# Kernel optimization log

Measured on AMD Instinct MI355X. Metric: run time of the kernel, lower is better.

Reference implementation:

```python
import jax, jax.numpy as jnp
import numpy as np

NEG_SLOPE = 0.01  # F.leaky_relu default
DROP_P = 0.5      # F.dropout(p=0.5, training=True by default in this code)


def _lrelu(x):
    return jnp.where(x >= 0, x, NEG_SLOPE * x)


def _hconv(Xi, X, Ht, Hs, edge_w, theta, w_trans, bias):
    # Faithful to Ht.T @ diag(edge_w) @ Hs @ X @ theta + Xi @ w_trans + bias,
    # with diag(edge_w) fused as a per-row scale of the [E, out] intermediate.
    msg = (Hs @ X) @ theta                 # [E, out]
    agg = Ht.T @ (edge_w[:, None] * msg)   # [N, out]
    return _lrelu(agg + Xi @ w_trans + bias)


def setup_inputs() -> dict:
    key = jax.random.key(0)
    ks = jax.random.split(key, 14)
    N, E, F0, H = 8192, 4096, 128, 128
    f32 = jnp.float32
    return {
        "xi": jax.random.normal(ks[0], (N, F0), f32),
        "x": jax.random.normal(ks[1], (N, F0), f32),
        "Ht": jax.random.uniform(ks[2], (E, N), f32),
        "Hs": jax.random.uniform(ks[3], (E, N), f32),
        "state": jax.random.normal(ks[4], (N, 1), f32),
        # conv0 params (std=0.01 init as in torch code)
        "w_trans0": 0.01 * jax.random.normal(ks[5], (F0, H), f32),
        "theta0": 0.01 * jax.random.normal(ks[6], (F0, H), f32),
        "edge_w0": jnp.ones((E,), f32),
        "bias0": 0.01 * jax.random.normal(ks[7], (H,), f32),
        # conv1 params
        "w_trans1": 0.01 * jax.random.normal(ks[8], (H, H), f32),
        "theta1": 0.01 * jax.random.normal(ks[9], (H, H), f32),
        "edge_w1": jnp.ones((E,), f32),
        "bias1": 0.01 * jax.random.normal(ks[10], (H,), f32),
        # fc: Linear(H+1, 1)
        "fc_w": 0.01 * jax.random.normal(ks[11], (H + 1, 1), f32),
        "fc_b": 0.01 * jax.random.normal(ks[12], (1,), f32),
    }


def reference(xi, x, Ht, Hs, state,
              w_trans0, theta0, edge_w0, bias0,
              w_trans1, theta1, edge_w1, bias1,
              fc_w, fc_b):
    X1 = _hconv(xi, x, Ht, Hs, edge_w0, theta0, w_trans0, bias0)  # [N, H]
    # F.dropout(p=0.5) is active (training=True default); fixed mask for determinism
    keep = jax.random.bernoulli(jax.random.key(42), 1.0 - DROP_P, X1.shape)
    X1 = jnp.where(keep, X1 / (1.0 - DROP_P), 0.0)
    X2 = _hconv(xi, X1, Ht, Hs, edge_w1, theta1, w_trans1, bias1)  # [N, H]
    X = _lrelu(X2)  # second leaky_relu, as in DQN.forward
    Xc = jnp.concatenate([X, state], axis=1)  # [N, H+1]
    return Xc @ fc_w + fc_b  # [N, 1]
```

## Files before the change

kernel.cpp:

```cpp
#include <hip/hip_runtime.h>
#include <stdint.h>


typedef short short8 __attribute__((ext_vector_type(8)));
typedef float f32x4 __attribute__((ext_vector_type(4)));

static constexpr int N = 8192, E = 4096, F = 128;
static constexpr int SA = 16, SB = 8;

#define ASM_VMCNT(n) asm volatile("s_waitcnt vmcnt(" #n ")" ::: "memory")
#define ASM_LGKM0() asm volatile("s_waitcnt lgkmcnt(0)" ::: "memory")

__device__ __forceinline__ void gload_lds16(const short* g, short* l) {
  __builtin_amdgcn_global_load_lds(
      (const __attribute__((address_space(1))) unsigned int*)g,
      (__attribute__((address_space(3))) unsigned int*)l, 16, 0, 0);
}

__device__ __forceinline__ unsigned rotl32(unsigned x, int r) {
  return (x << r) | (x >> (32 - r));
}

__device__ __forceinline__ uint2 threefry2x32(unsigned k0, unsigned k1,
                                              unsigned x0, unsigned x1) {
  unsigned ks[3] = {k0, k1, k0 ^ k1 ^ 0x1BD11BDAu};
  x0 += ks[0];
  x1 += ks[1];
  const int R0[4] = {13, 15, 26, 6};
  const int R1[4] = {17, 29, 16, 24};
#pragma unroll
  for (int i = 0; i < 5; ++i) {
#pragma unroll
    for (int j = 0; j < 4; ++j) {
      const int r = (i % 2 == 0) ? R0[j] : R1[j];
      x0 += x1;
      x1 = rotl32(x1, r);
      x1 ^= x0;
    }
    x0 += ks[(i + 1) % 3];
    x1 += ks[(i + 2) % 3] + (unsigned)(i + 1);
  }
  return make_uint2(x0, x1);
}

__device__ __forceinline__ float drop_scale(unsigned idx) {
  const uint2 o = threefry2x32(0u, 42u, 0u, idx);
  return ((o.x ^ o.y) & 0x80000000u) ? 0.0f : 2.0f;
}

__device__ __forceinline__ float lrelu(float v) {
  return v >= 0.0f ? v : 0.01f * v;
}

__device__ __forceinline__ unsigned rne1(float a) {
  unsigned ua = __builtin_bit_cast(unsigned, a);
  ua += 0x7fffu + ((ua >> 16) & 1u);
  return ua >> 16;
}
__device__ __forceinline__ float bf16_val(unsigned u16) {
  return __builtin_bit_cast(float, u16 << 16);
}
__device__ __forceinline__ unsigned pk_bf16(float a, float b) {
  return rne1(a) | (rne1(b) << 16);
}
__device__ __forceinline__ void split2(float a, float b, unsigned& hi,
                                       unsigned& lo) {
  const unsigned ha = rne1(a), hb = rne1(b);
  const float ra = a - bf16_val(ha), rb = b - bf16_val(hb);
  hi = ha | (hb << 16);
  lo = rne1(ra) | (rne1(rb) << 16);
}
__device__ __forceinline__ void split1(float a, unsigned& h, unsigned& l) {
  h = rne1(a);
  l = rne1(a - bf16_val(h));
}

template <bool TRANSA>
__global__ __launch_bounds__(512, 4) void big_gemm(
    const float* __restrict__ A, const short* __restrict__ Bhg,
    const short* __restrict__ Blg, float* __restrict__ P, int M, int lda) {
  __shared__ __align__(16) short As[3][4096];
  __shared__ __align__(16) short Bhs[3][4096];
  __shared__ __align__(16) short Bls[3][4096];

  const int tid = threadIdx.x;
  const int lane = tid & 63;
  const int w = tid >> 6;
  const int wm = (w & 3) << 5;
  const int wn = (w >> 2) << 6;
  const int l15 = lane & 15;
  const int q = lane >> 4;
  const int r0 = blockIdx.x * 128;
  constexpr int NT = 16;
  const int kt0 = blockIdx.y * NT;

  const int m0a = tid >> 3;
  const int m0b = (512 + tid) >> 3;
  const int kq0 = tid & 7;
  const int m1 = tid & 127;
  const int eo1 = tid >> 7;

  float Rf[2][8];

  auto loadA = [&](float* R, int kt) {
    if constexpr (!TRANSA) {
      *(float4*)&R[0] =
          *(const float4*)(A + (size_t)(r0 + m0a) * lda + kt * 32 + 4 * kq0);
      *(float4*)&R[4] =
          *(const float4*)(A + (size_t)(r0 + m0b) * lda + kt * 32 + 4 * kq0);
    } else {
#pragma unroll
      for (int r = 0; r < 8; ++r)
        R[r] = A[(size_t)(kt * 32 + 8 * eo1 + r) * lda + r0 + m1];
    }
  };
  auto packA = [&](const float* R, int buf) {
    if constexpr (!TRANSA) {
      const int s0 = (kq0 >> 1) ^ ((m0a >> 1) & 3);
      uint2 u0 = {pk_bf16(R[0], R[1]), pk_bf16(R[2], R[3])};
      *(uint2*)&As[buf][m0a * 32 + s0 * 8 + (kq0 & 1) * 4] = u0;
      const int s1 = (kq0 >> 1) ^ ((m0b >> 1) & 3);
      uint2 u1 = {pk_bf16(R[4], R[5]), pk_bf16(R[6], R[7])};
      *(uint2*)&As[buf][m0b * 32 + s1 * 8 + (kq0 & 1) * 4] = u1;
    } else {
      const int s0 = eo1 ^ ((m1 >> 1) & 3);
      uint4 u = {pk_bf16(R[0], R[1]), pk_bf16(R[2], R[3]),
                 pk_bf16(R[4], R[5]), pk_bf16(R[6], R[7])};
      *(uint4*)&As[buf][m1 * 32 + s0 * 8] = u;
    }
  };
  auto stageB = [&](int buf, int kt) {
    const size_t g = (size_t)kt * 4096 + w * 512 + lane * 8;
    gload_lds16(Bhg + g, &Bhs[buf][w * 512]);
    gload_lds16(Blg + g, &Bls[buf][w * 512]);
  };

  f32x4 acc[2][4];
#pragma unroll
  for (int i = 0; i < 2; ++i)
#pragma unroll
    for (int j = 0; j < 4; ++j) acc[i][j] = (f32x4){0.f, 0.f, 0.f, 0.f};

  loadA(Rf[0], kt0 + 0);
  stageB(0, kt0 + 0);
  loadA(Rf[1], kt0 + 1);
  stageB(1, kt0 + 1);
  if constexpr (!TRANSA) ASM_VMCNT(4); else ASM_VMCNT(10);
  __builtin_amdgcn_sched_barrier(0);
  packA(Rf[0], 0);
  ASM_LGKM0();
  __builtin_amdgcn_s_barrier();

  auto step = [&](int i, float* Ri, float* Rp) {
    const int cur = i % 3, nxt = (i + 1) % 3, nn = (i + 2) % 3;
    if (i + 2 < NT) {
      loadA(Ri, kt0 + i + 2);
      stageB(nn, kt0 + i + 2);
    }
    __builtin_amdgcn_sched_barrier(0);
    short8 af[2], bh[4], bl[4];
#pragma unroll
    for (int ii = 0; ii < 2; ++ii) {
      const int m = wm + 16 * ii + l15;
      af[ii] = *(const short8*)&As[cur][m * 32 + ((q ^ ((m >> 1) & 3)) << 3)];
    }
#pragma unroll
    for (int j = 0; j < 4; ++j) {
      const int c = wn + 16 * j + l15;
      bh[j] = *(const short8*)&Bhs[cur][c * 32 + (q << 3)];
      bl[j] = *(const short8*)&Bls[cur][c * 32 + (q << 3)];
    }
#pragma unroll
    for (int ii = 0; ii < 2; ++ii)
#pragma unroll
      for (int j = 0; j < 4; ++j) {
        acc[ii][j] = __builtin_amdgcn_mfma_f32_16x16x32_bf16(af[ii], bl[j],
                                                             acc[ii][j], 0, 0, 0);
        acc[ii][j] = __builtin_amdgcn_mfma_f32_16x16x32_bf16(af[ii], bh[j],
                                                             acc[ii][j], 0, 0, 0);
      }
    if (i + 1 < NT) {
      if (i + 2 < NT) {
        if constexpr (!TRANSA) ASM_VMCNT(4); else ASM_VMCNT(10);
      } else {
        ASM_VMCNT(0);
      }
      __builtin_amdgcn_sched_barrier(0);
      packA(Rp, nxt);
    }
    ASM_LGKM0();
    __builtin_amdgcn_s_barrier();
  };

  for (int ib = 0; ib < NT; ib += 2) {
    step(ib, Rf[0], Rf[1]);
    step(ib + 1, Rf[1], Rf[0]);
  }

  const int s = blockIdx.y;
  const int rquad = q << 2;
#pragma unroll
  for (int i = 0; i < 2; ++i)
#pragma unroll
    for (int j = 0; j < 4; ++j)
#pragma unroll
      for (int r = 0; r < 4; ++r) {
        const int row = r0 + wm + 16 * i + rquad + r;
        const int col = wn + 16 * j + l15;
        P[((size_t)s * M + row) * 128 + col] = acc[i][j][r];
      }
}

template <bool WA>
__device__ __forceinline__ void small_core(
    const float* __restrict__ src, const float* __restrict__ W,
    const float* __restrict__ bias, float* __restrict__ out,
    short* __restrict__ outH, short* __restrict__ outL, short* WTh, short* WTl,
    short* Xh, short* Xl, int n0, int tid) {
  constexpr int TI = WA ? 4 : 2;
  constexpr int TJ = WA ? 2 : 4;
  const int lane = tid & 63;
  const int w = tid >> 6;
  const int l15 = lane & 15;
  const int wm = (w & 1) * (WA ? 64 : 32);
  const int wn = (w >> 1) * (WA ? 32 : 64);

  f32x4 acc[TI][TJ];
#pragma unroll
  for (int i = 0; i < TI; ++i)
#pragma unroll
    for (int j = 0; j < TJ; ++j) acc[i][j] = (f32x4){0.f, 0.f, 0.f, 0.f};

  for (int k0 = 0; k0 < 128; k0 += 32) {
#pragma unroll
    for (int i = 0; i < 2; ++i) {
      const int f = i * 256 + tid;
      const int c = f & 127;
      const int eo = f >> 7;
      uint4 uh, ul;
      unsigned* ph = (unsigned*)&uh;
      unsigned* pl = (unsigned*)&ul;
#pragma unroll
      for (int r = 0; r < 4; ++r) {
        const float a = W[(size_t)(k0 + 8 * eo + 2 * r) * 128 + c];
        const float b = W[(size_t)(k0 + 8 * eo + 2 * r + 1) * 128 + c];
        split2(a, b, ph[r], pl[r]);
      }
      *(uint4*)&WTh[c * 40 + 8 * eo] = uh;
      *(uint4*)&WTl[c * 40 + 8 * eo] = ul;
    }
#pragma unroll
    for (int i = 0; i < 2; ++i) {
      const int qq = i * 256 + tid;
      const int n = qq >> 3;
      const int kq = qq & 7;
      const float4 v =
          *(const float4*)(src + (size_t)(n0 + n) * 128 + k0 + 4 * kq);
      uint2 uh, ul;
      split2(v.x, v.y, uh.x, ul.x);
      split2(v.z, v.w, uh.y, ul.y);
      *(uint2*)&Xh[n * 40 + 4 * kq] = uh;
      *(uint2*)&Xl[n * 40 + 4 * kq] = ul;
    }
    __syncthreads();

    const int koff = (lane >> 4) << 3;
    short8 ah[TI], al[TI], bh[TJ], bl[TJ];
#pragma unroll
    for (int i = 0; i < TI; ++i) {
      const int m = wm + 16 * i + l15;
      ah[i] = WA ? *(const short8*)&WTh[m * 40 + koff]
                 : *(const short8*)&Xh[m * 40 + koff];
      al[i] = WA ? *(const short8*)&WTl[m * 40 + koff]
                 : *(const short8*)&Xl[m * 40 + koff];
    }
#pragma unroll
    for (int j = 0; j < TJ; ++j) {
      const int c = wn + 16 * j + l15;
      bh[j] = WA ? *(const short8*)&Xh[c * 40 + koff]
                 : *(const short8*)&WTh[c * 40 + koff];
      bl[j] = WA ? *(const short8*)&Xl[c * 40 + koff]
                 : *(const short8*)&WTl[c * 40 + koff];
    }
#pragma unroll
    for (int i = 0; i < TI; ++i)
#pragma unroll
      for (int j = 0; j < TJ; ++j) {
        acc[i][j] = __builtin_amdgcn_mfma_f32_16x16x32_bf16(al[i], bh[j],
                                                            acc[i][j], 0, 0, 0);
        acc[i][j] = __builtin_amdgcn_mfma_f32_16x16x32_bf16(ah[i], bl[j],
                                                            acc[i][j], 0, 0, 0);
        acc[i][j] = __builtin_amdgcn_mfma_f32_16x16x32_bf16(ah[i], bh[j],
                                                            acc[i][j], 0, 0, 0);
      }
    __syncthreads();
  }

  const int rquad = (lane >> 4) << 2;
#pragma unroll
  for (int i = 0; i < TI; ++i)
#pragma unroll
    for (int j = 0; j < TJ; ++j) {
      if constexpr (WA) {
        const int colg = n0 + wn + 16 * j + l15;
        const size_t tb = (size_t)(colg >> 5) * 4096 + (colg & 31);
#pragma unroll
        for (int r = 0; r < 4; ++r) {
          const int row = wm + 16 * i + rquad + r;
          unsigned h, l;
          split1(acc[i][j][r], h, l);
          outH[tb + (size_t)row * 32] = (short)h;
          outL[tb + (size_t)row * 32] = (short)l;
        }
      } else {
#pragma unroll
        for (int r = 0; r < 4; ++r) {
          const int row = wm + 16 * i + rquad + r;
          const int col = wn + 16 * j + l15;
          out[(size_t)(n0 + row) * 128 + col] = acc[i][j][r] + bias[col];
        }
      }
    }
}

__global__ __launch_bounds__(256) void small_fused(
    const float* __restrict__ srcT, const float* __restrict__ Wth,
    const float* __restrict__ srcB, const float* __restrict__ Wwt,
    const float* __restrict__ bias, short* __restrict__ TtH,
    short* __restrict__ TtL, float* __restrict__ Badd) {
  __shared__ __align__(16) short WTh[128 * 40], WTl[128 * 40];
  __shared__ __align__(16) short Xh[64 * 40], Xl[64 * 40];
  const int n0 = blockIdx.x * 64;
  if (blockIdx.y == 0)
    small_core<true>(srcT, Wth, nullptr, nullptr, TtH, TtL, WTh, WTl, Xh, Xl,
                     n0, threadIdx.x);
  else
    small_core<false>(srcB, Wwt, bias, Badd, nullptr, nullptr, WTh, WTl, Xh, Xl,
                      n0, threadIdx.x);
}

__global__ __launch_bounds__(256) void reduce_A(const float* __restrict__ P,
                                                const float* __restrict__ ew,
                                                short* __restrict__ MtH,
                                                short* __restrict__ MtL) {
  __shared__ float Lt[8 * 132];
  const int tid = threadIdx.x;
  const int e0 = blockIdx.x * 8;
  {
    const int el = tid >> 5;
    const int cq = tid & 31;
    float4 a = {0.f, 0.f, 0.f, 0.f};
#pragma unroll
    for (int s = 0; s < SA; ++s) {
      const float4 v =
          *(const float4*)(P + ((size_t)s * E + e0 + el) * 128 + 4 * cq);
      a.x += v.x; a.y += v.y; a.z += v.z; a.w += v.w;
    }
    const float sc = ew[e0 + el];
    a.x *= sc; a.y *= sc; a.z *= sc; a.w *= sc;
    *(float4*)&Lt[el * 132 + 4 * cq] = a;
  }
  __syncthreads();
  {
    const int c = tid >> 1;
    const int eq = tid & 1;
    const int eb = e0 + 4 * eq;
    float4 o;
    o.x = Lt[(4 * eq + 0) * 132 + c];
    o.y = Lt[(4 * eq + 1) * 132 + c];
    o.z = Lt[(4 * eq + 2) * 132 + c];
    o.w = Lt[(4 * eq + 3) * 132 + c];
    uint2 uh, ul;
    split2(o.x, o.y, uh.x, ul.x);
    split2(o.z, o.w, uh.y, ul.y);
    const size_t off = (size_t)(eb >> 5) * 4096 + (size_t)c * 32 + (eb & 31);
    *(uint2*)&MtH[off] = uh;
    *(uint2*)&MtL[off] = ul;
  }
}

__global__ __launch_bounds__(256) void reduce_B1(const float* __restrict__ P,
                                                 const float* __restrict__ Badd,
                                                 float* __restrict__ X1) {
  const int q = blockIdx.x * 256 + threadIdx.x;
  const int n = q >> 5;
  const int cq = q & 31;
  float4 a = {0.f, 0.f, 0.f, 0.f};
#pragma unroll
  for (int s = 0; s < SB; ++s) {
    const float4 v = *(const float4*)(P + ((size_t)s * N + n) * 128 + 4 * cq);
    a.x += v.x; a.y += v.y; a.z += v.z; a.w += v.w;
  }
  const float4 b = *(const float4*)(Badd + (size_t)n * 128 + 4 * cq);
  const unsigned fb = (unsigned)(n * 128 + 4 * cq);
  float4 o;
  o.x = lrelu(a.x + b.x) * drop_scale(fb + 0u);
  o.y = lrelu(a.y + b.y) * drop_scale(fb + 1u);
  o.z = lrelu(a.z + b.z) * drop_scale(fb + 2u);
  o.w = lrelu(a.w + b.w) * drop_scale(fb + 3u);
  *(float4*)&X1[(size_t)n * 128 + 4 * cq] = o;
}

__global__ __launch_bounds__(256) void reduce_B2(
    const float* __restrict__ P, const float* __restrict__ Badd,
    const float* __restrict__ fcw, const float* __restrict__ state,
    const float* __restrict__ fcb, float* __restrict__ out) {
  __shared__ float part[4];
  const int tid = threadIdx.x;
  const int nn = tid >> 7;
  const int c = tid & 127;
  const int n = blockIdx.x * 2 + nn;
  float v = 0.f;
#pragma unroll
  for (int s = 0; s < SB; ++s) v += P[((size_t)s * N + n) * 128 + c];
  v += Badd[(size_t)n * 128 + c];
  float p = lrelu(lrelu(v)) * fcw[c];
#pragma unroll
  for (int m = 32; m >= 1; m >>= 1) p += __shfl_xor(p, m, 64);
  if ((tid & 63) == 0) part[tid >> 6] = p;
  __syncthreads();
  if (tid < 2)
    out[blockIdx.x * 2 + tid] = part[2 * tid] + part[2 * tid + 1] +
                                state[blockIdx.x * 2 + tid] * fcw[128] + fcb[0];
}

extern "C" void kernel_launch(void* const* d_in, const int* in_sizes, int n_in,
                              void* d_out, int out_size, void* d_ws,
                              size_t ws_size, hipStream_t stream) {
  (void)in_sizes; (void)n_in; (void)out_size; (void)ws_size;

  const float* xi = (const float*)d_in[0];
  const float* x = (const float*)d_in[1];
  const float* Ht = (const float*)d_in[2];
  const float* Hs = (const float*)d_in[3];
  const float* state = (const float*)d_in[4];
  const float* wt0 = (const float*)d_in[5];
  const float* th0 = (const float*)d_in[6];
  const float* ew0 = (const float*)d_in[7];
  const float* bi0 = (const float*)d_in[8];
  const float* wt1 = (const float*)d_in[9];
  const float* th1 = (const float*)d_in[10];
  const float* ew1 = (const float*)d_in[11];
  const float* bi1 = (const float*)d_in[12];
  const float* fcw = (const float*)d_in[13];
  const float* fcb = (const float*)d_in[14];
  float* out = (float*)d_out;

  float* ws = (float*)d_ws;
  float* P = ws;
  short* TtH = (short*)(P + (size_t)8388608);
  short* TtL = TtH + (size_t)1048576;
  short* MtH = TtL + (size_t)1048576;
  short* MtL = MtH + (size_t)524288;
  float* Badd = (float*)(MtL + (size_t)524288);
  float* X1 = Badd + (size_t)N * 128;

  small_fused<<<dim3(N / 64, 2), 256, 0, stream>>>(x, th0, xi, wt0, bi0, TtH,
                                                   TtL, Badd);
  big_gemm<false><<<dim3(E / 128, SA), 512, 0, stream>>>(Hs, TtH, TtL, P, E, N);
  reduce_A<<<E / 8, 256, 0, stream>>>(P, ew0, MtH, MtL);
  big_gemm<true><<<dim3(N / 128, SB), 512, 0, stream>>>(Ht, MtH, MtL, P, N, N);
  reduce_B1<<<N * F / 4 / 256, 256, 0, stream>>>(P, Badd, X1);

  small_fused<<<dim3(N / 64, 2), 256, 0, stream>>>(X1, th1, xi, wt1, bi1, TtH,
                                                   TtL, Badd);
  big_gemm<false><<<dim3(E / 128, SA), 512, 0, stream>>>(Hs, TtH, TtL, P, E, N);
  reduce_A<<<E / 8, 256, 0, stream>>>(P, ew1, MtH, MtL);
  big_gemm<true><<<dim3(N / 128, SB), 512, 0, stream>>>(Ht, MtH, MtL, P, N, N);
  reduce_B2<<<N / 2, 256, 0, stream>>>(P, Badd, fcw, state, fcb, out);
}
```

Before: 458.2 us.

## Load A fragments directly into registers and re-layout B tiles by k-quarter

The big GEMM no longer stages the A operand through shared memory. Each lane loads its own fp32 A fragment straight from global memory into a triple-buffered register set and packs it to bf16 just before the MFMAs. This removes the LDS writes, the LDS reads and the lgkmcnt waits for A. The B hi/lo tiles produced by the small kernels are re-laid out so each k-quarter is contiguous, which lets the B fragment reads skip the swizzle. MFMA blocks are wrapped in s_setprio. In exchange it uses more registers, and the uncoalesced transposed-A global loads (8 strided scalar loads per row group) may hurt bandwidth.

```diff
diff --git a/kernel.cpp b/kernel.cpp
--- a/kernel.cpp
+++ b/kernel.cpp
@@ -9,7 +9,6 @@
 static constexpr int SA = 16, SB = 8;
 
 #define ASM_VMCNT(n) asm volatile("s_waitcnt vmcnt(" #n ")" ::: "memory")
-#define ASM_LGKM0() asm volatile("s_waitcnt lgkmcnt(0)" ::: "memory")
 
 __device__ __forceinline__ void gload_lds16(const short* g, short* l) {
   __builtin_amdgcn_global_load_lds(
@@ -79,7 +78,6 @@
 __global__ __launch_bounds__(512, 4) void big_gemm(
     const float* __restrict__ A, const short* __restrict__ Bhg,
     const short* __restrict__ Blg, float* __restrict__ P, int M, int lda) {
-  __shared__ __align__(16) short As[3][4096];
   __shared__ __align__(16) short Bhs[3][4096];
   __shared__ __align__(16) short Bls[3][4096];
 
@@ -94,39 +92,26 @@
   constexpr int NT = 16;
   const int kt0 = blockIdx.y * NT;
 
-  const int m0a = tid >> 3;
-  const int m0b = (512 + tid) >> 3;
-  const int kq0 = tid & 7;
-  const int m1 = tid & 127;
-  const int eo1 = tid >> 7;
-
-  float Rf[2][8];
-
-  auto loadA = [&](float* R, int kt) {
+  const int am0 = wm + l15;
+  const int am1 = wm + 16 + l15;
+
+  float Ra[3][16];
+
+  auto loadA = [&](int set, int kt) {
     if constexpr (!TRANSA) {
-      *(float4*)&R[0] =
-          *(const float4*)(A + (size_t)(r0 + m0a) * lda + kt * 32 + 4 * kq0);
-      *(float4*)&R[4] =
-          *(const float4*)(A + (size_t)(r0 + m0b) * lda + kt * 32 + 4 * kq0);
+      const float* p0 = A + (size_t)(r0 + am0) * lda + kt * 32 + q * 8;
+      const float* p1 = A + (size_t)(r0 + am1) * lda + kt * 32 + q * 8;
+      *(float4*)&Ra[set][0] = *(const float4*)p0;
+      *(float4*)&Ra[set][4] = *(const float4*)(p0 + 4);
+      *(float4*)&Ra[set][8] = *(const float4*)p1;
+      *(float4*)&Ra[set][12] = *(const float4*)(p1 + 4);
     } else {
-#pragma unroll
-      for (int r = 0; r < 8; ++r)
-        R[r] = A[(size_t)(kt * 32 + 8 * eo1 + r) * lda + r0 + m1];
-    }
-  };
-  auto packA = [&](const float* R, int buf) {
-    if constexpr (!TRANSA) {
-      const int s0 = (kq0 >> 1) ^ ((m0a >> 1) & 3);
-      uint2 u0 = {pk_bf16(R[0], R[1]), pk_bf16(R[2], R[3])};
-      *(uint2*)&As[buf][m0a * 32 + s0 * 8 + (kq0 & 1) * 4] = u0;
-      const int s1 = (kq0 >> 1) ^ ((m0b >> 1) & 3);
-      uint2 u1 = {pk_bf16(R[4], R[5]), pk_bf16(R[6], R[7])};
-      *(uint2*)&As[buf][m0b * 32 + s1 * 8 + (kq0 & 1) * 4] = u1;
-    } else {
-      const int s0 = eo1 ^ ((m1 >> 1) & 3);
-      uint4 u = {pk_bf16(R[0], R[1]), pk_bf16(R[2], R[3]),
-                 pk_bf16(R[4], R[5]), pk_bf16(R[6], R[7])};
-      *(uint4*)&As[buf][m1 * 32 + s0 * 8] = u;
+      const float* p0 = A + (size_t)(kt * 32 + q * 8) * lda + r0 + am0;
+#pragma unroll
+      for (int r = 0; r < 8; ++r) Ra[set][r] = p0[(size_t)r * lda];
+      const float* p1 = p0 + 16;
+#pragma unroll
+      for (int r = 0; r < 8; ++r) Ra[set][8 + r] = p1[(size_t)r * lda];
     }
   };
   auto stageB = [&](int buf, int kt) {
@@ -134,6 +119,12 @@
     gload_lds16(Bhg + g, &Bhs[buf][w * 512]);
     gload_lds16(Blg + g, &Bls[buf][w * 512]);
   };
+  auto mk = [&](const float* R) {
+    union { unsigned u[4]; short8 s; } c;
+#pragma unroll
+    for (int t = 0; t < 4; ++t) c.u[t] = pk_bf16(R[2 * t], R[2 * t + 1]);
+    return c.s;
+  };
 
   f32x4 acc[2][4];
 #pragma unroll
@@ -141,60 +132,65 @@
 #pragma unroll
     for (int j = 0; j < 4; ++j) acc[i][j] = (f32x4){0.f, 0.f, 0.f, 0.f};
 
-  loadA(Rf[0], kt0 + 0);
+  loadA(0, kt0 + 0);
   stageB(0, kt0 + 0);
-  loadA(Rf[1], kt0 + 1);
+  loadA(1, kt0 + 1);
   stageB(1, kt0 + 1);
-  if constexpr (!TRANSA) ASM_VMCNT(4); else ASM_VMCNT(10);
+  if constexpr (!TRANSA) ASM_VMCNT(4); else ASM_VMCNT(18);
   __builtin_amdgcn_sched_barrier(0);
-  packA(Rf[0], 0);
-  ASM_LGKM0();
   __builtin_amdgcn_s_barrier();
 
-  auto step = [&](int i, float* Ri, float* Rp) {
-    const int cur = i % 3, nxt = (i + 1) % 3, nn = (i + 2) % 3;
+#pragma unroll
+  for (int i = 0; i < NT; ++i) {
+    const int cur = i % 3;
     if (i + 2 < NT) {
-      loadA(Ri, kt0 + i + 2);
-      stageB(nn, kt0 + i + 2);
+      loadA((i + 2) % 3, kt0 + i + 2);
+      stageB((i + 2) % 3, kt0 + i + 2);
     }
     __builtin_amdgcn_sched_barrier(0);
-    short8 af[2], bh[4], bl[4];
-#pragma unroll
-    for (int ii = 0; ii < 2; ++ii) {
-      const int m = wm + 16 * ii + l15;
-      af[ii] = *(const short8*)&As[cur][m * 32 + ((q ^ ((m >> 1) & 3)) << 3)];
-    }
+
+    const short8 af0 = mk(&Ra[cur][0]);
+    const short8 af1 = mk(&Ra[cur][8]);
+
+    short8 bf[4];
 #pragma unroll
     for (int j = 0; j < 4; ++j) {
       const int c = wn + 16 * j + l15;
-      bh[j] = *(const short8*)&Bhs[cur][c * 32 + (q << 3)];
-      bl[j] = *(const short8*)&Bls[cur][c * 32 + (q << 3)];
-    }
-#pragma unroll
-    for (int ii = 0; ii < 2; ++ii)
-#pragma unroll
-      for (int j = 0; j < 4; ++j) {
-        acc[ii][j] = __builtin_amdgcn_mfma_f32_16x16x32_bf16(af[ii], bl[j],
-                                                             acc[ii][j], 0, 0, 0);
-        acc[ii][j] = __builtin_amdgcn_mfma_f32_16x16x32_bf16(af[ii], bh[j],
-                                                             acc[ii][j], 0, 0, 0);
-      }
+      bf[j] = *(const short8*)&Bls[cur][(q << 10) + c * 8];
+    }
+    __builtin_amdgcn_s_setprio(1);
+#pragma unroll
+    for (int j = 0; j < 4; ++j) {
+      acc[0][j] =
+          __builtin_amdgcn_mfma_f32_16x16x32_bf16(af0, bf[j], acc[0][j], 0, 0, 0);
+      acc[1][j] =
+          __builtin_amdgcn_mfma_f32_16x16x32_bf16(af1, bf[j], acc[1][j], 0, 0, 0);
+    }
+    __builtin_amdgcn_s_setprio(0);
+#pragma unroll
+    for (int j = 0; j < 4; ++j) {
+      const int c = wn + 16 * j + l15;
+      bf[j] = *(const short8*)&Bhs[cur][(q << 10) + c * 8];
+    }
+    __builtin_amdgcn_s_setprio(1);
+#pragma unroll
+    for (int j = 0; j < 4; ++j) {
+      acc[0][j] =
+          __builtin_amdgcn_mfma_f32_16x16x32_bf16(af0, bf[j], acc[0][j], 0, 0, 0);
+      acc[1][j] =
+          __builtin_amdgcn_mfma_f32_16x16x32_bf16(af1, bf[j], acc[1][j], 0, 0, 0);
+    }
+    __builtin_amdgcn_s_setprio(0);
+
     if (i + 1 < NT) {
       if (i + 2 < NT) {
-        if constexpr (!TRANSA) ASM_VMCNT(4); else ASM_VMCNT(10);
+        if constexpr (!TRANSA) ASM_VMCNT(4); else ASM_VMCNT(18);
       } else {
         ASM_VMCNT(0);
       }
       __builtin_amdgcn_sched_barrier(0);
-      packA(Rp, nxt);
-    }
-    ASM_LGKM0();
-    __builtin_amdgcn_s_barrier();
-  };
-
-  for (int ib = 0; ib < NT; ib += 2) {
-    step(ib, Rf[0], Rf[1]);
-    step(ib + 1, Rf[1], Rf[0]);
+      __builtin_amdgcn_s_barrier();
+    }
   }
 
   const int s = blockIdx.y;
@@ -303,14 +299,15 @@
     for (int j = 0; j < TJ; ++j) {
       if constexpr (WA) {
         const int colg = n0 + wn + 16 * j + l15;
-        const size_t tb = (size_t)(colg >> 5) * 4096 + (colg & 31);
+        const size_t tb = (size_t)(colg >> 5) * 4096 +
+                          (size_t)(((colg & 31) >> 3)) * 1024 + (colg & 7);
 #pragma unroll
         for (int r = 0; r < 4; ++r) {
           const int row = wm + 16 * i + rquad + r;
           unsigned h, l;
           split1(acc[i][j][r], h, l);
-          outH[tb + (size_t)row * 32] = (short)h;
-          outL[tb + (size_t)row * 32] = (short)l;
+          outH[tb + (size_t)row * 8] = (short)h;
+          outL[tb + (size_t)row * 8] = (short)l;
         }
       } else {
 #pragma unroll
@@ -373,7 +370,9 @@
     uint2 uh, ul;
     split2(o.x, o.y, uh.x, ul.x);
     split2(o.z, o.w, uh.y, ul.y);
-    const size_t off = (size_t)(eb >> 5) * 4096 + (size_t)c * 32 + (eb & 31);
+    const size_t off = (size_t)(eb >> 5) * 4096 +
+                       (size_t)(((eb & 31) >> 3)) * 1024 + (size_t)c * 8 +
+                       (eb & 7);
     *(uint2*)&MtH[off] = uh;
     *(uint2*)&MtL[off] = ul;
   }
```

New measurement: 473.3 us. +3.3%, slower.
